# Performance work log

Measured on AMD Instinct MI355X. Metric: run time of the kernel, lower is better.

## Reference

```python
import jax, jax.numpy as jnp
import numpy as np

D_MODEL = 1024
N_HEADS = 16
D_K = D_MODEL // N_HEADS
BATCH = 4
SEQ = 2048


def setup_inputs() -> dict:
    key = jax.random.key(0)
    ks = jax.random.split(key, 12)
    s = 1.0 / np.sqrt(D_MODEL)
    inp = {
        "context_sequence": jax.random.normal(ks[0], (BATCH, SEQ, D_MODEL), jnp.float32),
        "value_sequence": jax.random.normal(ks[1], (BATCH, SEQ, D_MODEL), jnp.float32),
        # True = masked (causal: cannot attend to future positions)
        "mask": jnp.triu(jnp.ones((SEQ, SEQ), dtype=bool), k=1),
        "Wq": jax.random.uniform(ks[2], (D_MODEL, D_MODEL), jnp.float32, -s, s),
        "bq": jax.random.uniform(ks[3], (D_MODEL,), jnp.float32, -s, s),
        "Wk": jax.random.uniform(ks[4], (D_MODEL, D_MODEL), jnp.float32, -s, s),
        "bk": jax.random.uniform(ks[5], (D_MODEL,), jnp.float32, -s, s),
        "Wv": jax.random.uniform(ks[6], (D_MODEL, D_MODEL), jnp.float32, -s, s),
        "bv": jax.random.uniform(ks[7], (D_MODEL,), jnp.float32, -s, s),
        "Wo": jax.random.uniform(ks[8], (D_MODEL, D_MODEL), jnp.float32, -s, s),
        "bo": jax.random.uniform(ks[9], (D_MODEL,), jnp.float32, -s, s),
    }
    return inp


def reference(context_sequence, value_sequence, mask, Wq, bq, Wk, bk, Wv, bv, Wo, bo):
    B, S, _ = context_sequence.shape
    # projections; split heads: [B, H, S, Dk]
    def split_heads(x):
        return x.reshape(B, S, N_HEADS, D_K).transpose(0, 2, 1, 3)

    Q = split_heads(context_sequence @ Wq + bq)
    K = split_heads(context_sequence @ Wk + bk)
    V = split_heads(value_sequence @ Wv + bv)

    scale = 1.0 / jnp.sqrt(jnp.asarray(D_K, dtype=Q.dtype))
    scores = jnp.einsum("bhqd,bhkd->bhqk", Q, K) * scale  # [B,H,S,S]
    scores = jnp.where(mask, jnp.asarray(-1e9, dtype=scores.dtype), scores)
    attn = jax.nn.softmax(scores, axis=-1)
    out = jnp.einsum("bhqk,bhkd->bhqd", attn, V)
    out = out.transpose(0, 2, 1, 3).reshape(B, S, D_MODEL)
    return out @ Wo + bo  # dropout p=0 (eval) -> identity
```

## Files before the change

kernel.cpp:

```cpp
#include <hip/hip_runtime.h>
#include <stdint.h>

#define D_MODEL 1024
#define SEQ 2048
#define BATCH 4
#define NH 16
#define DK 64

typedef float f32x4 __attribute__((ext_vector_type(4)));
typedef float f32x16 __attribute__((ext_vector_type(16)));
typedef __bf16 bf16x8 __attribute__((ext_vector_type(8)));
typedef unsigned short us4v __attribute__((ext_vector_type(4)));

__device__ __forceinline__ unsigned short f2bf(float f) {
  union { float f; unsigned u; } x; x.f = f;
  unsigned r = x.u + 0x7FFFu + ((x.u >> 16) & 1u);
  return (unsigned short)(r >> 16);
}

__device__ __forceinline__ void gll16(const void* g, void* l) {
  __builtin_amdgcn_global_load_lds(
      (__attribute__((address_space(1))) void*)g,
      (__attribute__((address_space(3))) void*)l, 16, 0, 0);
}

__device__ __forceinline__ int cvtpk(float lo, float hi) {
  int r;
  asm("v_cvt_pk_bf16_f32 %0, %1, %2" : "=v"(r) : "v"(lo), "v"(hi));
  return r;
}
__device__ __forceinline__ void pl32swap(int& a, int& b) {
  asm volatile("v_permlane32_swap_b32 %0, %1" : "+v"(a), "+v"(b));
}

__global__ void cvtbf(const float* __restrict__ in, unsigned short* __restrict__ out, const int n) {
  const int t = blockIdx.x * blockDim.x + threadIdx.x;
  const int stride = gridDim.x * blockDim.x;
  for (int i = t * 4; i < n; i += stride * 4) {
    const float4 v = *(const float4*)&in[i];
    us4v o;
    o[0] = f2bf(v.x); o[1] = f2bf(v.y); o[2] = f2bf(v.z); o[3] = f2bf(v.w);
    *(us4v*)&out[i] = o;
  }
}

__global__ void wtrans(const float* __restrict__ W0, const float* __restrict__ W1,
                       const float* __restrict__ W2, const float* __restrict__ W3,
                       unsigned short* __restrict__ T0, unsigned short* __restrict__ T1,
                       unsigned short* __restrict__ T2, unsigned short* __restrict__ T3) {
  __shared__ float t[32][33];
  const int z = blockIdx.z;
  const float* W = (z == 0) ? W0 : (z == 1) ? W1 : (z == 2) ? W2 : W3;
  unsigned short* T = (z == 0) ? T0 : (z == 1) ? T1 : (z == 2) ? T2 : T3;
  const int n0 = blockIdx.x * 32, k0 = blockIdx.y * 32;
  const int tx = threadIdx.x, ty = threadIdx.y;
#pragma unroll
  for (int i = 0; i < 4; ++i)
    t[ty + 8 * i][tx] = W[(size_t)(k0 + ty + 8 * i) * D_MODEL + n0 + tx];
  __syncthreads();
#pragma unroll
  for (int i = 0; i < 4; ++i)
    T[(size_t)(n0 + ty + 8 * i) * D_MODEL + k0 + tx] = f2bf(t[tx][ty + 8 * i]);
}

__global__ __launch_bounds__(256) void gemm128(
    const unsigned short* __restrict__ A, const unsigned short* __restrict__ Bt,
    const float* __restrict__ bias, unsigned short* __restrict__ outb,
    float* __restrict__ outf, const int mode) {
  __shared__ __align__(16) unsigned short Alds[2 * 128 * 64];
  __shared__ __align__(16) unsigned short Blds[2 * 128 * 64];
  const int tid = threadIdx.x;
  const int lane = tid & 63;
  const int w = tid >> 6;
  const int wr = w >> 1, wc = w & 1;

  int flat = (int)blockIdx.x + 8 * (int)blockIdx.y;
  flat = (flat & 7) * 64 + (flat >> 3);
  const int n0 = (flat & 7) * 128;
  const int m0 = (flat >> 3) * 128;

  const int srow = tid >> 3, sslot = tid & 7;

  auto stage = [&](int kk, int buf) {
#pragma unroll
    for (int i = 0; i < 4; ++i) {
      const int r = srow + 32 * i;
      const int gc = kk * 64 + ((sslot ^ (r & 7)) << 3);
      gll16(A + (size_t)(m0 + r) * D_MODEL + gc, &Alds[buf * 8192 + tid * 8 + i * 2048]);
      gll16(Bt + (size_t)(n0 + r) * D_MODEL + gc, &Blds[buf * 8192 + tid * 8 + i * 2048]);
    }
  };

  f32x4 acc[4][4] = {};

  stage(0, 0);
  stage(1, 1);

  const int NK = D_MODEL / 64;
  for (int kk = 0; kk < NK; ++kk) {
    const int cur = kk & 1;
    if (kk + 1 < NK) asm volatile("s_waitcnt vmcnt(8)" ::: "memory");
    else             asm volatile("s_waitcnt vmcnt(0)" ::: "memory");
    __builtin_amdgcn_s_barrier();
    asm volatile("" ::: "memory");

    const unsigned short* Al = &Alds[cur * 8192];
    const unsigned short* Bl = &Blds[cur * 8192];
#pragma unroll
    for (int kf = 0; kf < 2; ++kf) {
      const int sb = kf * 4 + (lane >> 4);
      bf16x8 a[4], b[4];
#pragma unroll
      for (int m = 0; m < 4; ++m) {
        const int row = wr * 64 + m * 16 + (lane & 15);
        a[m] = *(const bf16x8*)&Al[row * 64 + ((sb ^ (row & 7)) << 3)];
      }
#pragma unroll
      for (int n = 0; n < 4; ++n) {
        const int row = wc * 64 + n * 16 + (lane & 15);
        b[n] = *(const bf16x8*)&Bl[row * 64 + ((sb ^ (row & 7)) << 3)];
      }
#pragma unroll
      for (int m = 0; m < 4; ++m)
#pragma unroll
        for (int n = 0; n < 4; ++n)
          acc[m][n] = __builtin_amdgcn_mfma_f32_16x16x32_bf16(a[m], b[n], acc[m][n], 0, 0, 0);
    }

    asm volatile("" ::: "memory");
    __builtin_amdgcn_s_barrier();

    if (kk + 2 < NK) stage(kk + 2, cur);
  }

#pragma unroll
  for (int m = 0; m < 4; ++m) {
    const int rb = m0 + wr * 64 + m * 16 + ((lane >> 4) << 2);
#pragma unroll
    for (int n = 0; n < 4; ++n) {
      const int col = n0 + wc * 64 + n * 16 + (lane & 15);
      const float bv = bias[col];
#pragma unroll
      for (int j = 0; j < 4; ++j) {
        const int row = rb + j;
        const float v = acc[m][n][j] + bv;
        if (mode == 2) {
          outf[(size_t)row * D_MODEL + col] = v;
        } else {
          const int b_ = row >> 11, s_ = row & (SEQ - 1);
          const int h_ = col >> 6, d_ = col & (DK - 1);
          size_t idx;
          if (mode == 0) idx = (((size_t)(b_ * NH + h_)) * SEQ + s_) * DK + d_;
          else           idx = (((size_t)(b_ * NH + h_)) * DK + d_) * SEQ + s_;
          outb[idx] = f2bf(v);
        }
      }
    }
  }
}

__global__ __launch_bounds__(256, 4) void attn4w(
    const unsigned short* __restrict__ Q, const unsigned short* __restrict__ K,
    const unsigned short* __restrict__ Vt, unsigned short* __restrict__ O) {
  __shared__ __align__(16) unsigned short Klds[2 * 64 * 64];
  __shared__ __align__(16) unsigned short Vlds[2 * 64 * 64];

  const int tid = threadIdx.x, lane = tid & 63, w = tid >> 6;
  const int lq = lane & 31, hi = lane >> 5;
  const int bh = blockIdx.x;
  const int strip = 15 - (int)blockIdx.y;
  const size_t qkbase = (size_t)bh * SEQ * DK;
  const size_t vbase = (size_t)bh * DK * SEQ;
  const int srow = tid >> 3, sslot = tid & 7;
  const int b_ = bh >> 4, h_ = bh & (NH - 1);

  const int q0 = strip * 128;
  const int qw0 = q0 + w * 32;
  const int qg = qw0 + lq;
  const int n = 2 * strip + 2;

  bf16x8 qb[4];
  {
    const unsigned short* qp = Q + qkbase + (size_t)qg * DK + hi * 8;
#pragma unroll
    for (int ks = 0; ks < 4; ++ks) {
      qb[ks] = *(const bf16x8*)(qp + ks * 16);
#pragma unroll
      for (int e = 0; e < 8; ++e)
        qb[ks][e] = (__bf16)((float)qb[ks][e] * 0.125f);
    }
  }

  float m = -3e38f, l = 0.f;
  f32x16 o0 = {}, o1 = {};

#pragma unroll
  for (int i = 0; i < 2; ++i) {
    const int r = srow + 32 * i;
    const int sc = (sslot ^ (r & 7)) << 3;
    gll16(K + qkbase + (size_t)r * DK + sc, &Klds[tid * 8 + i * 2048]);
    gll16(Vt + vbase + (size_t)r * SEQ + sc, &Vlds[tid * 8 + i * 2048]);
  }
#pragma unroll
  for (int i = 0; i < 2; ++i) {
    const int r = srow + 32 * i;
    const int sc = (sslot ^ (r & 7)) << 3;
    gll16(K + qkbase + (size_t)(64 + r) * DK + sc, &Klds[4096 + tid * 8 + i * 2048]);
    gll16(Vt + vbase + (size_t)r * SEQ + 64 + sc, &Vlds[4096 + tid * 8 + i * 2048]);
  }

  for (int jt = 0; jt < n; ++jt) {
    const int cur = jt & 1;
    if (jt + 1 < n) asm volatile("s_waitcnt vmcnt(4)" ::: "memory");
    else            asm volatile("s_waitcnt vmcnt(0)" ::: "memory");
    __builtin_amdgcn_s_barrier();
    asm volatile("" ::: "memory");

    if (64 * jt < qw0 + 32) {
      const unsigned short* Kl = &Klds[cur * 4096];
      const unsigned short* Vl = &Vlds[cur * 4096];

      f32x16 st0 = {}, st1 = {};
      __builtin_amdgcn_s_setprio(1);
#pragma unroll
      for (int ks = 0; ks < 4; ++ks) {
        const int so = ((ks * 2 + hi) ^ (lq & 7)) << 3;
        const bf16x8 ka0 = *(const bf16x8*)&Kl[lq * 64 + so];
        const bf16x8 ka1 = *(const bf16x8*)&Kl[(32 + lq) * 64 + so];
        st0 = __builtin_amdgcn_mfma_f32_32x32x16_bf16(ka0, qb[ks], st0, 0, 0, 0);
        st1 = __builtin_amdgcn_mfma_f32_32x32x16_bf16(ka1, qb[ks], st1, 0, 0, 0);
      }
      __builtin_amdgcn_s_setprio(0);

      if (64 * jt + 63 > qw0) {
        const int rb = 64 * jt + 4 * hi - qg;
#pragma unroll
        for (int r = 0; r < 16; ++r) {
          const int crow0 = (r & 3) + 8 * (r >> 2);
          if (crow0 + rb > 0)      st0[r] = -3e38f;
          if (crow0 + 32 + rb > 0) st1[r] = -3e38f;
        }
      }

      float tmax[8];
#pragma unroll
      for (int r = 0; r < 8; ++r)
        tmax[r] = fmaxf(fmaxf(st0[r], st0[r + 8]), fmaxf(st1[r], st1[r + 8]));
      float mx = fmaxf(fmaxf(fmaxf(tmax[0], tmax[1]), fmaxf(tmax[2], tmax[3])),
                       fmaxf(fmaxf(tmax[4], tmax[5]), fmaxf(tmax[6], tmax[7])));
      mx = fmaxf(mx, __shfl_xor(mx, 32));

      if (__any((int)(mx > m + 8.0f))) {
        const float mnew = fmaxf(m, mx);
        const float alpha = exp2f((m - mnew) * 1.44269504f);
        m = mnew;
        l *= alpha;
#pragma unroll
        for (int r = 0; r < 16; ++r) { o0[r] *= alpha; o1[r] *= alpha; }
      }

      const float ml = m * 1.44269504f;
#pragma unroll
      for (int r = 0; r < 16; ++r) {
        st0[r] = exp2f(__builtin_fmaf(st0[r], 1.44269504f, -ml));
        st1[r] = exp2f(__builtin_fmaf(st1[r], 1.44269504f, -ml));
      }

      float tsum[8];
#pragma unroll
      for (int r = 0; r < 8; ++r)
        tsum[r] = (st0[r] + st0[r + 8]) + (st1[r] + st1[r + 8]);
      float rs = ((tsum[0] + tsum[1]) + (tsum[2] + tsum[3])) +
                 ((tsum[4] + tsum[5]) + (tsum[6] + tsum[7]));
      rs += __shfl_xor(rs, 32);
      l += rs;

      bf16x8 pb[4];
#pragma unroll
      for (int ks = 0; ks < 4; ++ks) {
        const int base = (ks & 1) * 8;
        float p0, p1, p2, p3, p4, p5, p6, p7;
        if (ks < 2) {
          p0 = st0[base + 0]; p1 = st0[base + 1]; p2 = st0[base + 2]; p3 = st0[base + 3];
          p4 = st0[base + 4]; p5 = st0[base + 5]; p6 = st0[base + 6]; p7 = st0[base + 7];
        } else {
          p0 = st1[base + 0]; p1 = st1[base + 1]; p2 = st1[base + 2]; p3 = st1[base + 3];
          p4 = st1[base + 4]; p5 = st1[base + 5]; p6 = st1[base + 6]; p7 = st1[base + 7];
        }
        int a0 = cvtpk(p0, p1), a1 = cvtpk(p2, p3);
        int a2 = cvtpk(p4, p5), a3 = cvtpk(p6, p7);
        pl32swap(a0, a2);
        pl32swap(a1, a3);
        union { int i[4]; bf16x8 v; } u;
        u.i[0] = a0; u.i[1] = a1; u.i[2] = a2; u.i[3] = a3;
        pb[ks] = u.v;
      }

      __builtin_amdgcn_s_setprio(1);
#pragma unroll
      for (int ks = 0; ks < 4; ++ks) {
        const int so = ((ks * 2 + hi) ^ (lq & 7)) << 3;
        const bf16x8 va0 = *(const bf16x8*)&Vl[lq * 64 + so];
        const bf16x8 va1 = *(const bf16x8*)&Vl[(32 + lq) * 64 + so];
        o0 = __builtin_amdgcn_mfma_f32_32x32x16_bf16(va0, pb[ks], o0, 0, 0, 0);
        o1 = __builtin_amdgcn_mfma_f32_32x32x16_bf16(va1, pb[ks], o1, 0, 0, 0);
      }
      __builtin_amdgcn_s_setprio(0);
    }

    asm volatile("" ::: "memory");
    __builtin_amdgcn_s_barrier();

    if (jt + 2 < n) {
      const int kv0 = (jt + 2) * 64;
#pragma unroll
      for (int i = 0; i < 2; ++i) {
        const int r = srow + 32 * i;
        const int sc = (sslot ^ (r & 7)) << 3;
        gll16(K + qkbase + (size_t)(kv0 + r) * DK + sc,
              &Klds[cur * 4096 + tid * 8 + i * 2048]);
        gll16(Vt + vbase + (size_t)r * SEQ + kv0 + sc,
              &Vlds[cur * 4096 + tid * 8 + i * 2048]);
      }
    }
  }

  const float rl = 1.0f / l;
  unsigned short* orow = O + (size_t)(b_ * SEQ + qg) * D_MODEL + h_ * DK;
#pragma unroll
  for (int g = 0; g < 4; ++g) {
    us4v pk0, pk1;
#pragma unroll
    for (int j = 0; j < 4; ++j) {
      pk0[j] = f2bf(o0[4 * g + j] * rl);
      pk1[j] = f2bf(o1[4 * g + j] * rl);
    }
    const int d0 = 8 * g + 4 * hi;
    *(us4v*)&orow[d0] = pk0;
    *(us4v*)&orow[32 + d0] = pk1;
  }
}

extern "C" void kernel_launch(void* const* d_in, const int* in_sizes, int n_in,
                              void* d_out, int out_size, void* d_ws, size_t ws_size,
                              hipStream_t stream) {
  const float* ctx = (const float*)d_in[0];
  const float* val = (const float*)d_in[1];
  const float* Wq = (const float*)d_in[3];
  const float* bq = (const float*)d_in[4];
  const float* Wk = (const float*)d_in[5];
  const float* bk = (const float*)d_in[6];
  const float* Wv = (const float*)d_in[7];
  const float* bv = (const float*)d_in[8];
  const float* Wo = (const float*)d_in[9];
  const float* bo = (const float*)d_in[10];

  unsigned short* ws = (unsigned short*)d_ws;
  const size_t XSZ = (size_t)BATCH * SEQ * D_MODEL;
  const size_t WSZ = (size_t)D_MODEL * D_MODEL;
  unsigned short* Xc  = ws;
  unsigned short* Xv  = Xc + XSZ;
  unsigned short* Wqt = Xv + XSZ;
  unsigned short* Wkt = Wqt + WSZ;
  unsigned short* Wvt = Wkt + WSZ;
  unsigned short* Wot = Wvt + WSZ;
  unsigned short* Qb  = Wot + WSZ;
  unsigned short* Kb  = Qb + XSZ;
  unsigned short* Vtb = Kb + XSZ;
  unsigned short* Ob  = Vtb + XSZ;

  cvtbf<<<1024, 256, 0, stream>>>(ctx, Xc, (int)XSZ);
  cvtbf<<<1024, 256, 0, stream>>>(val, Xv, (int)XSZ);
  wtrans<<<dim3(32, 32, 4), dim3(32, 8), 0, stream>>>(Wq, Wk, Wv, Wo, Wqt, Wkt, Wvt, Wot);

  dim3 gg(D_MODEL / 128, BATCH * SEQ / 128);
  gemm128<<<gg, 256, 0, stream>>>(Xc, Wqt, bq, Qb, nullptr, 0);
  gemm128<<<gg, 256, 0, stream>>>(Xc, Wkt, bk, Kb, nullptr, 0);
  gemm128<<<gg, 256, 0, stream>>>(Xv, Wvt, bv, Vtb, nullptr, 1);

  attn4w<<<dim3(BATCH * NH, 16), 256, 0, stream>>>(Qb, Kb, Vtb, Ob);

  gemm128<<<gg, 256, 0, stream>>>(Ob, Wot, bo, nullptr, (float*)d_out, 2);
}
```

Measured before the change: 195.3 us.

## Fuse Q/K projections into one GEMM, merge input casts, fold log2e into Q scale

The Q and K projections now run as one GEMM over the concatenated Wq|Wk (which are adjacent in the workspace), with per-column bias and output selection. The two input cast kernels are merged into one launch, and the block-swizzle is generalized to the grid size. In attention, log2(e) is folded into the Q prescale so softmax uses raw v_exp_f32 with no per-element FMA, and the rescale threshold is adjusted to match. This trades small launch and ALU overheads for slightly different rounding from the bf16 scaling of Q.

```diff
diff --git a/kernel.cpp b/kernel.cpp
--- a/kernel.cpp
+++ b/kernel.cpp
@@ -32,12 +32,19 @@
 __device__ __forceinline__ void pl32swap(int& a, int& b) {
   asm volatile("v_permlane32_swap_b32 %0, %1" : "+v"(a), "+v"(b));
 }
-
-__global__ void cvtbf(const float* __restrict__ in, unsigned short* __restrict__ out, const int n) {
+__device__ __forceinline__ float exp2fast(float x) {
+  float r;
+  asm("v_exp_f32 %0, %1" : "=v"(r) : "v"(x));
+  return r;
+}
+
+__global__ void cvtbf2(const float* __restrict__ a, const float* __restrict__ b,
+                       unsigned short* __restrict__ out, const int nseg) {
   const int t = blockIdx.x * blockDim.x + threadIdx.x;
   const int stride = gridDim.x * blockDim.x;
-  for (int i = t * 4; i < n; i += stride * 4) {
-    const float4 v = *(const float4*)&in[i];
+  for (int i = t * 4; i < 2 * nseg; i += stride * 4) {
+    const float* src = (i < nseg) ? &a[i] : &b[i - nseg];
+    const float4 v = *(const float4*)src;
     us4v o;
     o[0] = f2bf(v.x); o[1] = f2bf(v.y); o[2] = f2bf(v.z); o[3] = f2bf(v.w);
     *(us4v*)&out[i] = o;
@@ -65,7 +72,8 @@
 
 __global__ __launch_bounds__(256) void gemm128(
     const unsigned short* __restrict__ A, const unsigned short* __restrict__ Bt,
-    const float* __restrict__ bias, unsigned short* __restrict__ outb,
+    const float* __restrict__ bias, const float* __restrict__ bias2,
+    unsigned short* __restrict__ outb, unsigned short* __restrict__ outb2,
     float* __restrict__ outf, const int mode) {
   __shared__ __align__(16) unsigned short Alds[2 * 128 * 64];
   __shared__ __align__(16) unsigned short Blds[2 * 128 * 64];
@@ -74,10 +82,13 @@
   const int w = tid >> 6;
   const int wr = w >> 1, wc = w & 1;
 
-  int flat = (int)blockIdx.x + 8 * (int)blockIdx.y;
-  flat = (flat & 7) * 64 + (flat >> 3);
-  const int n0 = (flat & 7) * 128;
-  const int m0 = (flat >> 3) * 128;
+  const int nbn = (int)gridDim.x;
+  const int chunk = (nbn * (int)gridDim.y) >> 3;
+  const int nbs = __builtin_ctz(nbn);
+  int flat = (int)blockIdx.x + nbn * (int)blockIdx.y;
+  flat = (flat & 7) * chunk + (flat >> 3);
+  const int n0 = (flat & (nbn - 1)) * 128;
+  const int m0 = (flat >> nbs) * 128;
 
   const int srow = tid >> 3, sslot = tid & 7;
 
@@ -139,7 +150,10 @@
 #pragma unroll
     for (int n = 0; n < 4; ++n) {
       const int col = n0 + wc * 64 + n * 16 + (lane & 15);
-      const float bv = bias[col];
+      const int colw = col & (D_MODEL - 1);
+      const float bv = (mode == 0)
+                           ? ((col < D_MODEL) ? bias[colw] : bias2[colw])
+                           : bias[col];
 #pragma unroll
       for (int j = 0; j < 4; ++j) {
         const int row = rb + j;
@@ -148,11 +162,17 @@
           outf[(size_t)row * D_MODEL + col] = v;
         } else {
           const int b_ = row >> 11, s_ = row & (SEQ - 1);
-          const int h_ = col >> 6, d_ = col & (DK - 1);
+          const int h_ = colw >> 6, d_ = colw & (DK - 1);
           size_t idx;
-          if (mode == 0) idx = (((size_t)(b_ * NH + h_)) * SEQ + s_) * DK + d_;
-          else           idx = (((size_t)(b_ * NH + h_)) * DK + d_) * SEQ + s_;
-          outb[idx] = f2bf(v);
+          unsigned short* dst;
+          if (mode == 0) {
+            idx = (((size_t)(b_ * NH + h_)) * SEQ + s_) * DK + d_;
+            dst = (col < D_MODEL) ? outb : outb2;
+          } else {
+            idx = (((size_t)(b_ * NH + h_)) * DK + d_) * SEQ + s_;
+            dst = outb;
+          }
+          dst[idx] = f2bf(v);
         }
       }
     }
@@ -181,13 +201,14 @@
 
   bf16x8 qb[4];
   {
+    const float QSCALE = 0.125f * 1.44269504f;
     const unsigned short* qp = Q + qkbase + (size_t)qg * DK + hi * 8;
 #pragma unroll
     for (int ks = 0; ks < 4; ++ks) {
       qb[ks] = *(const bf16x8*)(qp + ks * 16);
 #pragma unroll
       for (int e = 0; e < 8; ++e)
-        qb[ks][e] = (__bf16)((float)qb[ks][e] * 0.125f);
+        qb[ks][e] = (__bf16)((float)qb[ks][e] * QSCALE);
     }
   }
 
@@ -250,20 +271,19 @@
                        fmaxf(fmaxf(tmax[4], tmax[5]), fmaxf(tmax[6], tmax[7])));
       mx = fmaxf(mx, __shfl_xor(mx, 32));
 
-      if (__any((int)(mx > m + 8.0f))) {
+      if (__any((int)(mx > m + 11.5416f))) {
         const float mnew = fmaxf(m, mx);
-        const float alpha = exp2f((m - mnew) * 1.44269504f);
+        const float alpha = exp2fast(m - mnew);
         m = mnew;
         l *= alpha;
 #pragma unroll
         for (int r = 0; r < 16; ++r) { o0[r] *= alpha; o1[r] *= alpha; }
       }
 
-      const float ml = m * 1.44269504f;
 #pragma unroll
       for (int r = 0; r < 16; ++r) {
-        st0[r] = exp2f(__builtin_fmaf(st0[r], 1.44269504f, -ml));
-        st1[r] = exp2f(__builtin_fmaf(st1[r], 1.44269504f, -ml));
+        st0[r] = exp2fast(st0[r] - m);
+        st1[r] = exp2fast(st1[r] - m);
       }
 
       float tsum[8];
@@ -369,16 +389,13 @@
   unsigned short* Vtb = Kb + XSZ;
   unsigned short* Ob  = Vtb + XSZ;
 
-  cvtbf<<<1024, 256, 0, stream>>>(ctx, Xc, (int)XSZ);
-  cvtbf<<<1024, 256, 0, stream>>>(val, Xv, (int)XSZ);
+  cvtbf2<<<2048, 256, 0, stream>>>(ctx, val, Xc, (int)XSZ);
   wtrans<<<dim3(32, 32, 4), dim3(32, 8), 0, stream>>>(Wq, Wk, Wv, Wo, Wqt, Wkt, Wvt, Wot);
 
-  dim3 gg(D_MODEL / 128, BATCH * SEQ / 128);
-  gemm128<<<gg, 256, 0, stream>>>(Xc, Wqt, bq, Qb, nullptr, 0);
-  gemm128<<<gg, 256, 0, stream>>>(Xc, Wkt, bk, Kb, nullptr, 0);
-  gemm128<<<gg, 256, 0, stream>>>(Xv, Wvt, bv, Vtb, nullptr, 1);
+  gemm128<<<dim3(16, 64), 256, 0, stream>>>(Xc, Wqt, bq, bk, Qb, Kb, nullptr, 0);
+  gemm128<<<dim3(8, 64), 256, 0, stream>>>(Xv, Wvt, bv, nullptr, Vtb, nullptr, nullptr, 1);
 
   attn4w<<<dim3(BATCH * NH, 16), 256, 0, stream>>>(Qb, Kb, Vtb, Ob);
 
-  gemm128<<<gg, 256, 0, stream>>>(Ob, Wot, bo, nullptr, (float*)d_out, 2);
-}
+  gemm128<<<dim3(8, 64), 256, 0, stream>>>(Ob, Wot, bo, nullptr, nullptr, nullptr, (float*)d_out, 2);
+}
```

Result: faster. 188.3 us (-3.6%).
